# Optimization experiments

Measured on AMD Instinct MI355X. Metric: run time of the kernel, lower is better.

The kernel has to match this reference:

```python
import jax, jax.numpy as jnp
import numpy as np

N = 50000   # nodes
E = 600000  # edges
D = 128     # in = hidden = out channels
L = 3       # num_layers
LN_EPS = 1e-5


def setup_inputs() -> dict:
    key = jax.random.key(0)
    ks = jax.random.split(key, 4)
    x = jax.random.normal(ks[0], (N, D), dtype=jnp.float32)
    edge_index = jax.random.randint(ks[1], (2, E), 0, N, dtype=jnp.int32)
    # GCNConv linear weights (glorot-ish scale) and biases, one per layer
    Ws = jax.random.normal(ks[2], (L, D, D), dtype=jnp.float32) / np.sqrt(D)
    bs = jnp.zeros((L, D), dtype=jnp.float32)
    # LayerNorm affine params per layer
    ln_w = jnp.ones((L, D), dtype=jnp.float32)
    ln_b = jnp.zeros((L, D), dtype=jnp.float32)
    # PReLU (single shared slope per layer, torch default init 0.25)
    alphas = jnp.full((L,), 0.25, dtype=jnp.float32)
    return {"x": x, "edge_index": edge_index, "Ws": Ws, "bs": bs,
            "ln_w": ln_w, "ln_b": ln_b, "alphas": alphas}


def reference(x, edge_index, Ws, bs, ln_w, ln_b, alphas):
    # --- gcn_norm: add self-loops, symmetric D^{-1/2} (A+I) D^{-1/2} ---
    loop = jnp.arange(N, dtype=edge_index.dtype)
    src = jnp.concatenate([edge_index[0], loop])  # [E+N]
    dst = jnp.concatenate([edge_index[1], loop])  # [E+N]
    deg = jax.ops.segment_sum(jnp.ones_like(dst, dtype=x.dtype), dst,
                              num_segments=N)
    dinv = jnp.where(deg > 0, jax.lax.rsqrt(jnp.maximum(deg, 1.0)), 0.0)
    norm = (dinv[src] * dinv[dst])[:, None]  # [E+N, 1]

    h = x
    for l in range(L):
        # GCNConv: linear -> gather -> scale -> scatter-add -> bias
        h = h @ Ws[l]                                   # [N, D]
        msg = h[src] * norm                             # [E+N, D]
        h = jax.ops.segment_sum(msg, dst, num_segments=N) + bs[l]
        # LayerNorm over feature dim
        mu = jnp.mean(h, axis=-1, keepdims=True)
        var = jnp.mean((h - mu) ** 2, axis=-1, keepdims=True)
        h = (h - mu) * jax.lax.rsqrt(var + LN_EPS) * ln_w[l] + ln_b[l]
        # PReLU
        h = jnp.where(h >= 0, h, alphas[l] * h)
    return h
```

## Files before the change

### kernel.cpp

```cpp
#include <hip/hip_runtime.h>
#include <hip/hip_bf16.h>

#define NN 50000
#define EE 600000
#define DD 128
#define LL 3
#define LN_EPS 1e-5f
#define CAP 64
#define CNTS 16
#define ALD 136
#define POOL 16
#define NTILES (NN / POOL)
#define FILLB ((EE + 255) / 256)

typedef __attribute__((ext_vector_type(8))) short short8;
typedef __attribute__((ext_vector_type(4))) float floatx4;
typedef __attribute__((ext_vector_type(4))) unsigned uintx4;

__device__ inline unsigned short f2bf(float f) {
    union { float f; unsigned u; } a; a.f = f;
    unsigned r = a.u + 0x7fffu + ((a.u >> 16) & 1u);
    return (unsigned short)(r >> 16);
}

__device__ inline uintx4 gload4(const unsigned short* p) {
    uintx4 r;
    asm volatile("global_load_dwordx4 %0, %1, off" : "=v"(r) : "v"(p));
    return r;
}


__global__ __launch_bounds__(256) void init_kernel(const float* __restrict__ W,
                                                   unsigned short* __restrict__ Wt,
                                                   int* __restrict__ cnt) {
    int tid = blockIdx.x * 256 + threadIdx.x;
    for (int i = tid; i < NN * CNTS / 4; i += gridDim.x * 256)
        ((int4*)cnt)[i] = make_int4(0, 0, 0, 0);
    for (int i = tid; i < LL * DD * DD; i += gridDim.x * 256) {
        int l = i >> 14, n = (i >> 7) & 127, k = i & 127;
        Wt[i] = f2bf(W[(l << 14) + k * DD + n]);
    }
}


__global__ __launch_bounds__(256) void fill_kernel(
    const int* __restrict__ src, const int* __restrict__ dst,
    int* __restrict__ cnt, int* __restrict__ csrc) {
    int e = blockIdx.x * 256 + threadIdx.x;
    if (e < EE) {
        int d = dst[e];
        int s = src[e];
        int pos = atomicAdd(&cnt[d * CNTS], 1);
        csrc[(size_t)d * CAP + pos] = s;
    }
}


__global__ __launch_bounds__(256) void gemm0_kernel(
    const float* __restrict__ A, const unsigned short* __restrict__ Wt,
    const int* __restrict__ cnt, unsigned short* __restrict__ Cb) {
    __shared__ unsigned short alds[POOL * ALD];
    __shared__ float s_dinv[POOL];
    int tid = threadIdx.x;
    int lane = tid & 63;
    int w = tid >> 6;
    int nodebase = blockIdx.x * POOL;

    if (tid < POOL)
        s_dinv[tid] = rsqrtf((float)(cnt[(nodebase + tid) * CNTS] + 1));

    {
        int row = tid >> 4;
        int kc = (tid & 15) * 8;
        const float* ap = &A[(size_t)(nodebase + row) * DD + kc];
        float4 v0 = *(const float4*)&ap[0];
        float4 v1 = *(const float4*)&ap[4];
        float fv[8] = {v0.x, v0.y, v0.z, v0.w, v1.x, v1.y, v1.z, v1.w};
        unsigned short uv[8];
        #pragma unroll
        for (int q = 0; q < 8; q++) uv[q] = f2bf(fv[q]);
        *(uint4*)&alds[row * ALD + kc] = *(uint4*)&uv[0];
    }
    __syncthreads();

    int cbase = w * 32;
    int kq = (lane >> 4) * 8;
    int mrow = lane & 15;
    floatx4 acc[2] = {{0.f,0.f,0.f,0.f},{0.f,0.f,0.f,0.f}};
    #pragma unroll
    for (int t = 0; t < 4; t++) {
        short8 a = *(const short8*)&alds[mrow * ALD + t * 32 + kq];
        #pragma unroll
        for (int j = 0; j < 2; j++) {
            short8 b = *(const short8*)&Wt[(cbase + j * 16 + (lane & 15)) * DD + t * 32 + kq];
            acc[j] = __builtin_amdgcn_mfma_f32_16x16x32_bf16(a, b, acc[j], 0, 0, 0);
        }
    }
    __syncthreads();

    {
        int r0 = (lane >> 4) * 4;
        #pragma unroll
        for (int i = 0; i < 4; i++) {
            float dvr = s_dinv[r0 + i];
            #pragma unroll
            for (int j = 0; j < 2; j++)
                alds[(r0 + i) * ALD + cbase + j * 16 + (lane & 15)] = f2bf(acc[j][i] * dvr);
        }
    }
    __syncthreads();
    {
        int srow = tid >> 4;
        int scol = (tid & 15) * 8;
        *(uint4*)&Cb[(size_t)(nodebase + srow) * DD + scol] =
            *(uint4*)&alds[srow * ALD + scol];
    }
}


__device__ inline void acc_row(float* acc, uintx4 t) {
    #pragma unroll
    for (int q = 0; q < 4; q++) {
        union { unsigned x; float f; } lo, hi;
        lo.x = t[q] << 16;
        hi.x = t[q] & 0xffff0000u;
        acc[2 * q]     += lo.f;
        acc[2 * q + 1] += hi.f;
    }
}

__device__ inline void agg_node(const unsigned short* __restrict__ Tb,
                                const int* __restrict__ cnt, const int* __restrict__ csrc,
                                const float* bv, const float* wv, const float* cv,
                                float alpha, int node, int f8, float* yv, float* dv_out) {
    int deg = cnt[node * CNTS];
    float dv = rsqrtf((float)(deg + 1));
    *dv_out = dv;
    const int* row = &csrc[(size_t)node * CAP];

    float acc[8] = {};
    acc_row(acc, *(const uintx4*)&Tb[((unsigned)node << 7) + f8]);

    int k = 0;
    for (; k + 4 <= deg; k += 4) {
        int4 ss = *(const int4*)&row[k];
        const unsigned short* p0 = &Tb[((unsigned)ss.x << 7) + f8];
        const unsigned short* p1 = &Tb[((unsigned)ss.y << 7) + f8];
        const unsigned short* p2 = &Tb[((unsigned)ss.z << 7) + f8];
        const unsigned short* p3 = &Tb[((unsigned)ss.w << 7) + f8];
        uintx4 t0 = gload4(p0);
        uintx4 t1 = gload4(p1);
        uintx4 t2 = gload4(p2);
        uintx4 t3 = gload4(p3);
        asm volatile("s_waitcnt vmcnt(0)" ::: "memory");
        __builtin_amdgcn_sched_barrier(0);
        acc_row(acc, t0); acc_row(acc, t1);
        acc_row(acc, t2); acc_row(acc, t3);
    }
    for (; k < deg; k++) {
        int s = row[k];
        acc_row(acc, *(const uintx4*)&Tb[((unsigned)s << 7) + f8]);
    }

    float a[8];
    float s1 = 0.f, s2 = 0.f;
    #pragma unroll
    for (int q = 0; q < 8; q++) {
        a[q] = fmaf(acc[q], dv, bv[q]);
        s1 += a[q]; s2 += a[q] * a[q];
    }
    #pragma unroll
    for (int off = 8; off > 0; off >>= 1) {
        s1 += __shfl_xor(s1, off, 16);
        s2 += __shfl_xor(s2, off, 16);
    }
    float mu = s1 * (1.f / DD);
    float var = s2 * (1.f / DD) - mu * mu;
    float rstd = rsqrtf(var + LN_EPS);
    #pragma unroll
    for (int q = 0; q < 8; q++) {
        float y = (a[q] - mu) * rstd * wv[q] + cv[q];
        yv[q] = (y >= 0.f) ? y : alpha * y;
    }
}


__global__ __launch_bounds__(256) void aggemm_kernel(
    const unsigned short* __restrict__ Tb, const int* __restrict__ cnt,
    const int* __restrict__ csrc,
    const float* __restrict__ bias, const float* __restrict__ lnw,
    const float* __restrict__ lnb, const float* __restrict__ alphas, int layer,
    const unsigned short* __restrict__ Wt, unsigned short* __restrict__ Tout) {
    __shared__ unsigned short alds[POOL * ALD];
    __shared__ float s_dinv[POOL];
    int tid = threadIdx.x;
    int g = tid >> 4;
    int lane16 = tid & 15;
    int f8 = lane16 * 8;
    int nodebase = blockIdx.x * POOL;

    float4 b0 = *(const float4*)&bias[f8];
    float4 b1 = *(const float4*)&bias[f8 + 4];
    float4 w0 = *(const float4*)&lnw[f8];
    float4 w1 = *(const float4*)&lnw[f8 + 4];
    float4 c0 = *(const float4*)&lnb[f8];
    float4 c1 = *(const float4*)&lnb[f8 + 4];
    float bv[8] = {b0.x, b0.y, b0.z, b0.w, b1.x, b1.y, b1.z, b1.w};
    float wv[8] = {w0.x, w0.y, w0.z, w0.w, w1.x, w1.y, w1.z, w1.w};
    float cv[8] = {c0.x, c0.y, c0.z, c0.w, c1.x, c1.y, c1.z, c1.w};
    float alpha = alphas[layer];

    {
        int node = nodebase + g;
        float yv[8], dv;
        agg_node(Tb, cnt, csrc, bv, wv, cv, alpha, node, f8, yv, &dv);
        if (lane16 == 0) s_dinv[g] = dv;
        unsigned short pv[8];
        #pragma unroll
        for (int q = 0; q < 8; q++) pv[q] = f2bf(yv[q]);
        *(uint4*)&alds[g * ALD + f8] = *(uint4*)&pv[0];
    }
    __syncthreads();

    int lane = tid & 63;
    int w = tid >> 6;
    int cbase = w * 32;
    int kq = (lane >> 4) * 8;
    int mrow = lane & 15;
    floatx4 acc[2] = {{0.f,0.f,0.f,0.f},{0.f,0.f,0.f,0.f}};
    #pragma unroll
    for (int t = 0; t < 4; t++) {
        short8 a = *(const short8*)&alds[mrow * ALD + t * 32 + kq];
        #pragma unroll
        for (int j = 0; j < 2; j++) {
            short8 b = *(const short8*)&Wt[(cbase + j * 16 + (lane & 15)) * DD + t * 32 + kq];
            acc[j] = __builtin_amdgcn_mfma_f32_16x16x32_bf16(a, b, acc[j], 0, 0, 0);
        }
    }
    __syncthreads();

    {
        int r0 = (lane >> 4) * 4;
        #pragma unroll
        for (int i = 0; i < 4; i++) {
            float dvr = s_dinv[r0 + i];
            #pragma unroll
            for (int j = 0; j < 2; j++)
                alds[(r0 + i) * ALD + cbase + j * 16 + (lane & 15)] = f2bf(acc[j][i] * dvr);
        }
    }
    __syncthreads();
    {
        int srow = tid >> 4;
        int scol = (tid & 15) * 8;
        *(uint4*)&Tout[(size_t)(nodebase + srow) * DD + scol] =
            *(uint4*)&alds[srow * ALD + scol];
    }
}


__global__ __launch_bounds__(256) void agg_final_kernel(
    const unsigned short* __restrict__ Tb, const int* __restrict__ cnt,
    const int* __restrict__ csrc,
    const float* __restrict__ bias, const float* __restrict__ lnw,
    const float* __restrict__ lnb, const float* __restrict__ alphas, int layer,
    float* __restrict__ out) {
    int g = threadIdx.x >> 4;
    int lane16 = threadIdx.x & 15;
    int f8 = lane16 * 8;
    int node = blockIdx.x * POOL + g;

    float4 b0 = *(const float4*)&bias[f8];
    float4 b1 = *(const float4*)&bias[f8 + 4];
    float4 w0 = *(const float4*)&lnw[f8];
    float4 w1 = *(const float4*)&lnw[f8 + 4];
    float4 c0 = *(const float4*)&lnb[f8];
    float4 c1 = *(const float4*)&lnb[f8 + 4];
    float bv[8] = {b0.x, b0.y, b0.z, b0.w, b1.x, b1.y, b1.z, b1.w};
    float wv[8] = {w0.x, w0.y, w0.z, w0.w, w1.x, w1.y, w1.z, w1.w};
    float cv[8] = {c0.x, c0.y, c0.z, c0.w, c1.x, c1.y, c1.z, c1.w};

    float yv[8], dv;
    agg_node(Tb, cnt, csrc, bv, wv, cv, alphas[layer], node, f8, yv, &dv);

    float* op = &out[(size_t)node * DD + f8];
    *(float4*)&op[0] = make_float4(yv[0], yv[1], yv[2], yv[3]);
    *(float4*)&op[4] = make_float4(yv[4], yv[5], yv[6], yv[7]);
}


extern "C" void kernel_launch(void* const* d_in, const int* in_sizes, int n_in,
                              void* d_out, int out_size, void* d_ws, size_t ws_size,
                              hipStream_t stream) {
    const float* x    = (const float*)d_in[0];
    const int*   ei   = (const int*)d_in[1];
    const float* Ws   = (const float*)d_in[2];
    const float* bs   = (const float*)d_in[3];
    const float* lnw  = (const float*)d_in[4];
    const float* lnb  = (const float*)d_in[5];
    const float* alphas = (const float*)d_in[6];
    float* out = (float*)d_out;

    const int* src = ei;
    const int* dst = ei + EE;

    char* ws = (char*)d_ws;
    size_t off = 0;
    auto alloc = [&](size_t bytes) -> void* {
        void* p = ws + off;
        off = (off + bytes + 255) & ~(size_t)255;
        return p;
    };
    int* cnt  = (int*)alloc((size_t)NN * CNTS * sizeof(int));
    int* csrc = (int*)alloc((size_t)NN * CAP * sizeof(int));
    unsigned short* wt    = (unsigned short*)alloc((size_t)LL * DD * DD * sizeof(unsigned short));
    unsigned short* tbufA = (unsigned short*)alloc((size_t)NN * DD * sizeof(unsigned short));
    unsigned short* tbufB = (unsigned short*)alloc((size_t)NN * DD * sizeof(unsigned short));

    init_kernel<<<512, 256, 0, stream>>>(Ws, wt, cnt);
    fill_kernel<<<FILLB, 256, 0, stream>>>(src, dst, cnt, csrc);
    gemm0_kernel<<<NTILES, 256, 0, stream>>>(x, wt, cnt, tbufA);

    aggemm_kernel<<<NTILES, 256, 0, stream>>>(tbufA, cnt, csrc,
                                              bs + 0 * DD, lnw + 0 * DD, lnb + 0 * DD,
                                              alphas, 0, wt + 1 * DD * DD, tbufB);
    aggemm_kernel<<<NTILES, 256, 0, stream>>>(tbufB, cnt, csrc,
                                              bs + 1 * DD, lnw + 1 * DD, lnb + 1 * DD,
                                              alphas, 1, wt + 2 * DD * DD, tbufA);
    agg_final_kernel<<<NTILES, 256, 0, stream>>>(tbufA, cnt, csrc,
                                                 bs + 2 * DD, lnw + 2 * DD, lnb + 2 * DD,
                                                 alphas, 2, out);
}
```

Measured before the change: 234.5 us.

## Prefetch first 16 neighbor rows with buffer loads and a zero padding row

Replaces global loads in the neighbor gather with buffer loads through a resource descriptor. The first 16 neighbors are issued unconditionally, with missing slots pointed at a zero-filled padding row, so several loads stay in flight behind staged vmcnt waits instead of draining after every 4. This hides gather latency for the typical degree (~12), at the cost of wasted loads for low-degree nodes and extra registers that may lower occupancy.

```diff
diff --git a/kernel.cpp b/kernel.cpp
--- a/kernel.cpp
+++ b/kernel.cpp
@@ -23,19 +23,41 @@
     return (unsigned short)(r >> 16);
 }
 
-__device__ inline uintx4 gload4(const unsigned short* p) {
+__device__ inline uintx4 make_srsrc(const void* p, unsigned bytes) {
+    unsigned long long a = (unsigned long long)p;
     uintx4 r;
-    asm volatile("global_load_dwordx4 %0, %1, off" : "=v"(r) : "v"(p));
+    r.x = (unsigned)a;
+    r.y = (unsigned)(a >> 32);
+    r.z = bytes;
+    r.w = 0x00020000u;
     return r;
 }
+
+__device__ inline uintx4 bload(uintx4 srsrc, unsigned voff) {
+    uintx4 r;
+    asm volatile("buffer_load_dwordx4 %0, %1, %2, 0 offen"
+                 : "=v"(r) : "v"(voff), "s"(srsrc));
+    return r;
+}
+
+#define WAITV(n) do { \
+    asm volatile("s_waitcnt vmcnt(" #n ")" ::: "memory"); \
+    __builtin_amdgcn_sched_barrier(0); \
+} while (0)
 
 
 __global__ __launch_bounds__(256) void init_kernel(const float* __restrict__ W,
                                                    unsigned short* __restrict__ Wt,
-                                                   int* __restrict__ cnt) {
+                                                   int* __restrict__ cnt,
+                                                   unsigned short* __restrict__ tbufA,
+                                                   unsigned short* __restrict__ tbufB) {
     int tid = blockIdx.x * 256 + threadIdx.x;
     for (int i = tid; i < NN * CNTS / 4; i += gridDim.x * 256)
         ((int4*)cnt)[i] = make_int4(0, 0, 0, 0);
+    for (int i = tid; i < 16 * DD / 2; i += gridDim.x * 256) {
+        ((int*)&tbufA[(size_t)NN * DD])[i] = 0;
+        ((int*)&tbufB[(size_t)NN * DD])[i] = 0;
+    }
     for (int i = tid; i < LL * DD * DD; i += gridDim.x * 256) {
         int l = i >> 14, n = (i >> 7) & 127, k = i & 127;
         Wt[i] = f2bf(W[(l << 14) + k * DD + n]);
@@ -129,7 +151,7 @@
     }
 }
 
-__device__ inline void agg_node(const unsigned short* __restrict__ Tb,
+__device__ inline void agg_node(uintx4 srsrc,
                                 const int* __restrict__ cnt, const int* __restrict__ csrc,
                                 const float* bv, const float* wv, const float* cv,
                                 float alpha, int node, int f8, float* yv, float* dv_out) {
@@ -137,29 +159,55 @@
     float dv = rsqrtf((float)(deg + 1));
     *dv_out = dv;
     const int* row = &csrc[(size_t)node * CAP];
+    unsigned vbase = (unsigned)f8 * 2u;
+
+    int4 i0 = *(const int4*)&row[0];
+    int4 i1 = *(const int4*)&row[4];
+    int4 i2 = *(const int4*)&row[8];
+    int4 i3 = *(const int4*)&row[12];
+    int idx[16] = {i0.x, i0.y, i0.z, i0.w, i1.x, i1.y, i1.z, i1.w,
+                   i2.x, i2.y, i2.z, i2.w, i3.x, i3.y, i3.z, i3.w};
+    unsigned voff[16];
+    #pragma unroll
+    for (int k = 0; k < 16; k++) {
+        int s = (k < deg) ? idx[k] : NN;
+        voff[k] = ((unsigned)s << 8) + vbase;
+    }
+    unsigned voffself = ((unsigned)node << 8) + vbase;
+
+    WAITV(0);
+    uintx4 ts = bload(srsrc, voffself);
+    uintx4 t0 = bload(srsrc, voff[0]),  t1 = bload(srsrc, voff[1]);
+    uintx4 t2 = bload(srsrc, voff[2]),  t3 = bload(srsrc, voff[3]);
+    uintx4 t4 = bload(srsrc, voff[4]),  t5 = bload(srsrc, voff[5]);
+    uintx4 t6 = bload(srsrc, voff[6]),  t7 = bload(srsrc, voff[7]);
 
     float acc[8] = {};
-    acc_row(acc, *(const uintx4*)&Tb[((unsigned)node << 7) + f8]);
-
-    int k = 0;
-    for (; k + 4 <= deg; k += 4) {
+    WAITV(8);
+    acc_row(acc, ts);
+    WAITV(4);
+    acc_row(acc, t0); acc_row(acc, t1); acc_row(acc, t2); acc_row(acc, t3);
+    uintx4 u0 = bload(srsrc, voff[8]),  u1 = bload(srsrc, voff[9]);
+    uintx4 u2 = bload(srsrc, voff[10]), u3 = bload(srsrc, voff[11]);
+    WAITV(4);
+    acc_row(acc, t4); acc_row(acc, t5); acc_row(acc, t6); acc_row(acc, t7);
+    uintx4 w0 = bload(srsrc, voff[12]), w1 = bload(srsrc, voff[13]);
+    uintx4 w2 = bload(srsrc, voff[14]), w3 = bload(srsrc, voff[15]);
+    WAITV(4);
+    acc_row(acc, u0); acc_row(acc, u1); acc_row(acc, u2); acc_row(acc, u3);
+    WAITV(0);
+    acc_row(acc, w0); acc_row(acc, w1); acc_row(acc, w2); acc_row(acc, w3);
+
+    for (int k = 16; k < deg; k += 4) {
         int4 ss = *(const int4*)&row[k];
-        const unsigned short* p0 = &Tb[((unsigned)ss.x << 7) + f8];
-        const unsigned short* p1 = &Tb[((unsigned)ss.y << 7) + f8];
-        const unsigned short* p2 = &Tb[((unsigned)ss.z << 7) + f8];
-        const unsigned short* p3 = &Tb[((unsigned)ss.w << 7) + f8];
-        uintx4 t0 = gload4(p0);
-        uintx4 t1 = gload4(p1);
-        uintx4 t2 = gload4(p2);
-        uintx4 t3 = gload4(p3);
-        asm volatile("s_waitcnt vmcnt(0)" ::: "memory");
-        __builtin_amdgcn_sched_barrier(0);
-        acc_row(acc, t0); acc_row(acc, t1);
-        acc_row(acc, t2); acc_row(acc, t3);
-    }
-    for (; k < deg; k++) {
-        int s = row[k];
-        acc_row(acc, *(const uintx4*)&Tb[((unsigned)s << 7) + f8]);
+        unsigned v0 = ((unsigned)ss.x << 8) + vbase;
+        unsigned v1 = ((unsigned)((k + 1 < deg) ? ss.y : NN) << 8) + vbase;
+        unsigned v2 = ((unsigned)((k + 2 < deg) ? ss.z : NN) << 8) + vbase;
+        unsigned v3 = ((unsigned)((k + 3 < deg) ? ss.w : NN) << 8) + vbase;
+        uintx4 a0 = bload(srsrc, v0), a1 = bload(srsrc, v1);
+        uintx4 a2 = bload(srsrc, v2), a3 = bload(srsrc, v3);
+        WAITV(0);
+        acc_row(acc, a0); acc_row(acc, a1); acc_row(acc, a2); acc_row(acc, a3);
     }
 
     float a[8];
@@ -199,6 +247,8 @@
     int f8 = lane16 * 8;
     int nodebase = blockIdx.x * POOL;
 
+    uintx4 srsrc = make_srsrc(Tb, (NN + 1) * DD * 2);
+
     float4 b0 = *(const float4*)&bias[f8];
     float4 b1 = *(const float4*)&bias[f8 + 4];
     float4 w0 = *(const float4*)&lnw[f8];
@@ -213,7 +263,7 @@
     {
         int node = nodebase + g;
         float yv[8], dv;
-        agg_node(Tb, cnt, csrc, bv, wv, cv, alpha, node, f8, yv, &dv);
+        agg_node(srsrc, cnt, csrc, bv, wv, cv, alpha, node, f8, yv, &dv);
         if (lane16 == 0) s_dinv[g] = dv;
         unsigned short pv[8];
         #pragma unroll
@@ -270,6 +320,8 @@
     int f8 = lane16 * 8;
     int node = blockIdx.x * POOL + g;
 
+    uintx4 srsrc = make_srsrc(Tb, (NN + 1) * DD * 2);
+
     float4 b0 = *(const float4*)&bias[f8];
     float4 b1 = *(const float4*)&bias[f8 + 4];
     float4 w0 = *(const float4*)&lnw[f8];
@@ -281,7 +333,7 @@
     float cv[8] = {c0.x, c0.y, c0.z, c0.w, c1.x, c1.y, c1.z, c1.w};
 
     float yv[8], dv;
-    agg_node(Tb, cnt, csrc, bv, wv, cv, alphas[layer], node, f8, yv, &dv);
+    agg_node(srsrc, cnt, csrc, bv, wv, cv, alphas[layer], node, f8, yv, &dv);
 
     float* op = &out[(size_t)node * DD + f8];
     *(float4*)&op[0] = make_float4(yv[0], yv[1], yv[2], yv[3]);
@@ -314,10 +366,10 @@
     int* cnt  = (int*)alloc((size_t)NN * CNTS * sizeof(int));
     int* csrc = (int*)alloc((size_t)NN * CAP * sizeof(int));
     unsigned short* wt    = (unsigned short*)alloc((size_t)LL * DD * DD * sizeof(unsigned short));
-    unsigned short* tbufA = (unsigned short*)alloc((size_t)NN * DD * sizeof(unsigned short));
-    unsigned short* tbufB = (unsigned short*)alloc((size_t)NN * DD * sizeof(unsigned short));
-
-    init_kernel<<<512, 256, 0, stream>>>(Ws, wt, cnt);
+    unsigned short* tbufA = (unsigned short*)alloc((size_t)(NN + 16) * DD * sizeof(unsigned short));
+    unsigned short* tbufB = (unsigned short*)alloc((size_t)(NN + 16) * DD * sizeof(unsigned short));
+
+    init_kernel<<<512, 256, 0, stream>>>(Ws, wt, cnt, tbufA, tbufB);
     fill_kernel<<<FILLB, 256, 0, stream>>>(src, dst, cnt, csrc);
     gemm0_kernel<<<NTILES, 256, 0, stream>>>(x, wt, cnt, tbufA);
 
```

Result: no change. 230.0 us, median of 2 (-1.9%).
